# Optimization experiments

Measured on AMD Instinct MI355X. Metric: run time of the kernel, lower is better.

## Reference

```python
import jax, jax.numpy as jnp
import numpy as np

N, C, G, M, E = 100000, 8, 8, 32, 1600000
EPS = 1e-8


def setup_inputs() -> dict:
    key = jax.random.key(0)
    k1, k2, k3, k4, k5 = jax.random.split(key, 5)
    x = jax.random.randint(k1, (N,), 0, M)
    prev_h = jax.random.uniform(k2, (N, C, G), dtype=jnp.float32)
    edge_index = jax.random.randint(k3, (2, E), 0, N)
    Q_neigh = jax.random.normal(k4, (C, C, G), dtype=jnp.float32) * 1.25
    B = jax.random.normal(k5, (C, M, G), dtype=jnp.float32) * 1.25
    return {"x": x, "prev_h": prev_h, "edge_index": edge_index,
            "Q_neigh": Q_neigh, "B": B}


def reference(x, prev_h, edge_index, Q_neigh, B):
    n = prev_h.shape[0]
    # softmax reparameterization (vectorized over n_gen)
    Qs = jax.nn.softmax(Q_neigh, axis=0)          # [C, C, G], columns sum to 1 over dim 0
    Bs = jax.nn.softmax(B, axis=1)                # [C, M, G], rows sum to 1 over M

    dst, src = edge_index[0], edge_index[1]
    neigh = prev_h[src]                            # [E, C, G] gather
    summed = jax.ops.segment_sum(neigh, dst, num_segments=n)            # [N, C, G]
    counts = jax.ops.segment_sum(jnp.ones((src.shape[0],), prev_h.dtype), dst,
                                 num_segments=n)                        # [N]
    aggr = summed / jnp.maximum(counts, 1.0)[:, None, None]             # scatter-mean, 0 for isolated nodes

    B_nodes = jnp.transpose(Bs[:, x], (1, 0, 2))[:, :, None, :]         # [N, C, 1, G]
    unnorm = B_nodes * (Qs[None, :, :, :] * aggr[:, None, :, :]) + EPS  # [N, C, C, G]

    denom = unnorm.sum(axis=(1, 2), keepdims=True)                      # [N, 1, 1, G]
    posterior_il = unnorm / denom
    posterior_i = posterior_il.sum(axis=2)                              # [N, C, G]
    likelihood = jnp.log(jnp.squeeze(denom, (1, 2)))                    # [N, G]
    return likelihood, posterior_i
```

## Files before the change

kernel.cpp:

```cpp
#include <hip/hip_runtime.h>

#define C_    8
#define G_    8
#define CG    64
#define CAP   48
#define CELL  56
#define BSPAN 256
#define SBLK  256
#define CVT   160
#define BG    512
#define Z1    2048
#define Z2    2048
#define ZTOT  4096
#define EPSF  1e-8f

__device__ __forceinline__ unsigned short bf16rne(float v) {
    unsigned u = __float_as_uint(v);
    return (unsigned short)((u + 0x7FFFu + ((u >> 16) & 1u)) >> 16);
}
__device__ __forceinline__ float bf16tof(unsigned short h) {
    return __uint_as_float((unsigned)h << 16);
}

__device__ __forceinline__ void zsum_block(int zgid, const float* __restrict__ Bmat,
                                           float* __restrict__ Z, int M) {
    if (zgid >= ZTOT) return;
    __shared__ float zpart[4][8];
    int c = zgid & 7, bx = zgid >> 3;
    const float4* B4 = (const float4*)(Bmat + (size_t)c * M * G_);
    const int total4 = M * 2;
    int tid = bx * 256 + threadIdx.x;
    const int zstride = (ZTOT / 8) * 256;
    float a0 = 0.f, a1 = 0.f, a2 = 0.f, a3 = 0.f;
    for (int f = tid; f < total4; f += zstride) {
        float4 v = B4[f];
        a0 += __expf(v.x); a1 += __expf(v.y); a2 += __expf(v.z); a3 += __expf(v.w);
    }
    #pragma unroll
    for (int m = 2; m <= 32; m <<= 1) {
        a0 += __shfl_xor(a0, m, 64);
        a1 += __shfl_xor(a1, m, 64);
        a2 += __shfl_xor(a2, m, 64);
        a3 += __shfl_xor(a3, m, 64);
    }
    int lane = threadIdx.x & 63, w = threadIdx.x >> 6;
    if (lane < 2) {
        int g0 = lane * 4;
        zpart[w][g0 + 0] = a0; zpart[w][g0 + 1] = a1;
        zpart[w][g0 + 2] = a2; zpart[w][g0 + 3] = a3;
    }
    __syncthreads();
    if (threadIdx.x < 8) {
        float s = zpart[0][threadIdx.x] + zpart[1][threadIdx.x]
                + zpart[2][threadIdx.x] + zpart[3][threadIdx.x];
        atomicAdd(&Z[c * G_ + threadIdx.x], s);
    }
}

__global__ void k_d1(const int* __restrict__ ei, int E, int npart,
                     int* __restrict__ counts, int* __restrict__ staging,
                     const float* __restrict__ prev_h, unsigned short* __restrict__ ph16,
                     int N, const float* __restrict__ Qn, float* __restrict__ Qs,
                     const int* __restrict__ x, unsigned short* __restrict__ blog16,
                     const float* __restrict__ Bmat, float* __restrict__ Z, int M) {
    int b = blockIdx.x;
    if (b < SBLK) {
        __shared__ int cur[512];
        for (int p = threadIdx.x; p < npart; p += 256) cur[p] = 0;
        __syncthreads();
        int chunk = (E + SBLK - 1) / SBLK;
        int lo = b * chunk, hi = min(E, lo + chunk);
        for (int e = lo + threadIdx.x; e < hi; e += 256) {
            int dst = ei[e], src = ei[E + e];
            int p = dst >> 8;
            int c = atomicAdd(&cur[p], 1);
            if (c < CELL) staging[(p * SBLK + b) * CELL + c] = ((dst & 255) << 23) | src;
        }
        __syncthreads();
        for (int p = threadIdx.x; p < npart; p += 256)
            counts[p * SBLK + b] = cur[p];
    } else if (b < SBLK + CVT) {
        int gid = (b - SBLK) * 256 + threadIdx.x;
        int total8 = N * 8;
        const int cstride = CVT * 256;
        for (int f = gid; f < total8; f += cstride) {
            const float4* s = (const float4*)(prev_h + (size_t)f * 8);
            float4 v0 = s[0], v1 = s[1];
            float vv[8] = {v0.x, v0.y, v0.z, v0.w, v1.x, v1.y, v1.z, v1.w};
            unsigned r[4];
            #pragma unroll
            for (int k = 0; k < 4; ++k)
                r[k] = (unsigned)bf16rne(vv[2 * k]) | ((unsigned)bf16rne(vv[2 * k + 1]) << 16);
            *(uint4*)(ph16 + (size_t)f * 8) = make_uint4(r[0], r[1], r[2], r[3]);
        }
    } else if (b == SBLK + CVT) {
        __shared__ float e[512];
        __shared__ float cs[64];
        int t = threadIdx.x;
        e[t] = __expf(Qn[t]); e[t + 256] = __expf(Qn[t + 256]);
        __syncthreads();
        if (t < 64) {
            float s = 0.f;
            #pragma unroll
            for (int i2 = 0; i2 < 8; ++i2) s += e[i2 * 64 + t];
            cs[t] = s;
        }
        __syncthreads();
        Qs[t] = e[t] / cs[t & 63];
        Qs[t + 256] = e[t + 256] / cs[t & 63];
    } else if (b < SBLK + CVT + 1 + BG) {
        int gidx = b - (SBLK + CVT + 1);
        int lane = threadIdx.x & 63, w = threadIdx.x >> 6;
        int i = lane >> 3, g = lane & 7;
        const int step = BG * 4 * 4;
        for (int n0 = (gidx * 4 + w) * 4; n0 < N; n0 += step) {
            int xs[4];
            #pragma unroll
            for (int k = 0; k < 4; ++k) xs[k] = (n0 + k < N) ? x[n0 + k] : 0;
            #pragma unroll
            for (int k = 0; k < 4; ++k)
                if (n0 + k < N)
                    blog16[(size_t)(n0 + k) * CG + lane] =
                        bf16rne(Bmat[((size_t)i * M + xs[k]) * G_ + g]);
        }
    } else {
        zsum_block(b - (SBLK + CVT + 1 + BG), Bmat, Z, M);
    }
}

__global__ void k_d2(const int* __restrict__ counts, const int* __restrict__ staging,
                     int* __restrict__ cnt, int* __restrict__ csr, int N, int npart,
                     const float* __restrict__ Bmat, float* __restrict__ Z, int M) {
    int b = blockIdx.x;
    if (b >= npart) { zsum_block(Z1 + (b - npart), Bmat, Z, M); return; }
    __shared__ int cl[BSPAN];
    __shared__ int csl[BSPAN * CAP];
    int t = threadIdx.x;
    cl[t] = 0;
    __syncthreads();
    int cnum = min(counts[b * SBLK + t], CELL);
    int cbase = (b * SBLK + t) * CELL;
    for (int j = 0; j < cnum; ++j) {
        int v = staging[cbase + j];
        int local = (unsigned)v >> 23;
        int src = v & 0x7FFFFF;
        int pos = atomicAdd(&cl[local], 1);
        if (pos < CAP) csl[local * CAP + pos] = src;
    }
    __syncthreads();
    int n = b * BSPAN + t;
    if (n < N) cnt[n] = cl[t];
    for (int idx = t; idx < BSPAN * CAP; idx += 256)
        csr[(size_t)b * (BSPAN * CAP) + idx] = csl[idx];
}

__global__ void k_ti(const unsigned short* __restrict__ ph16, const int* __restrict__ cnt,
                     const int* __restrict__ csr, const float* __restrict__ Qs,
                     const unsigned short* __restrict__ blog16,
                     const float* __restrict__ Z, float* __restrict__ out, int N) {
    int lane = threadIdx.x & 63, w = threadIdx.x >> 6;
    int i = lane >> 3, g = lane & 7;
    int base = blockIdx.x * 16 + w * 4;
    if (base >= N) return;
    float invZ = 1.f / Z[lane];
    int nk[4]; bool valid[4]; int deg[4], dl[4], nb[4];
    #pragma unroll
    for (int k = 0; k < 4; ++k) {
        int n = base + k;
        valid[k] = (n < N);
        nk[k] = valid[k] ? n : (N - 1);
    }
    #pragma unroll
    for (int k = 0; k < 4; ++k) {
        deg[k] = valid[k] ? cnt[nk[k]] : 0;
        dl[k]  = min(deg[k], CAP);
        nb[k]  = dl[k] >> 2;
    }
    float q[8];
    #pragma unroll
    for (int l = 0; l < 8; ++l) q[l] = Qs[i * 64 + l * 8 + g];
    float acc[4] = {0.f, 0.f, 0.f, 0.f};
    int nbmax = max(max(nb[0], nb[1]), max(nb[2], nb[3]));
    for (int q2 = 0; q2 < nbmax; ++q2) {
        #pragma unroll
        for (int k = 0; k < 4; ++k) {
            if (q2 < nb[k]) {
                int4 s4 = ((const int4*)(csr + (size_t)nk[k] * CAP))[q2];
                acc[k] += bf16tof(ph16[(s4.x << 6) | lane]);
                acc[k] += bf16tof(ph16[(s4.y << 6) | lane]);
                acc[k] += bf16tof(ph16[(s4.z << 6) | lane]);
                acc[k] += bf16tof(ph16[(s4.w << 6) | lane]);
            }
        }
    }
    #pragma unroll
    for (int k = 0; k < 4; ++k) {
        const int* crow = csr + (size_t)nk[k] * CAP;
        for (int e2 = nb[k] * 4; e2 < dl[k]; ++e2)
            acc[k] += bf16tof(ph16[(crow[e2] << 6) | lane]);
    }
    #pragma unroll
    for (int k = 0; k < 4; ++k) {
        float aggr = (deg[k] > 0) ? acc[k] / (float)deg[k] : 0.f;
        float ti = 0.f;
        #pragma unroll
        for (int l = 0; l < 8; ++l) ti += q[l] * __shfl(aggr, l * 8 + g, 64);
        float bl = bf16tof(blog16[(size_t)nk[k] * CG + lane]);
        float u = __expf(bl) * invZ * ti;
        float s = u;
        #pragma unroll
        for (int m = 8; m <= 32; m <<= 1) s += __shfl_xor(s, m, 64);
        float denom = s + 64.f * EPSF;
        if (valid[k]) {
            if (i == 0) out[nk[k] * G_ + g] = logf(denom);
            out[(size_t)N * G_ + (size_t)nk[k] * CG + lane] = (u + 8.f * EPSF) / denom;
        }
    }
}

extern "C" void kernel_launch(void* const* d_in, const int* in_sizes, int n_in,
                              void* d_out, int out_size, void* d_ws, size_t ws_size,
                              hipStream_t stream) {
    const int*   x      = (const int*)d_in[0];
    const float* prev_h = (const float*)d_in[1];
    const int*   ei     = (const int*)d_in[2];
    const float* Qn     = (const float*)d_in[3];
    const float* Bm     = (const float*)d_in[4];
    float* out = (float*)d_out;

    int N = in_sizes[0];
    int E = in_sizes[2] / 2;
    int M = in_sizes[4] / CG;
    int npart = (N + BSPAN - 1) / BSPAN;
    int nAggr = (N + 15) / 16;

    float* Z      = (float*)d_ws;
    float* Qs     = Z + 64;
    int*   counts = (int*)d_ws + 576;
    int*   cnt    = counts + npart * SBLK;
    int*   stag   = cnt + N;
    int*   csr    = stag + (size_t)npart * SBLK * CELL;
    unsigned short* ph16   = (unsigned short*)(csr + (size_t)npart * BSPAN * CAP);
    unsigned short* blog16 = ph16 + (size_t)N * CG;

    hipMemsetAsync(d_ws, 0, 64 * sizeof(float), stream);

    k_d1<<<SBLK + CVT + 1 + BG + Z1, 256, 0, stream>>>(
        ei, E, npart, counts, stag, prev_h, ph16, N, Qn, Qs, x, blog16, Bm, Z, M);
    k_d2<<<npart + Z2, 256, 0, stream>>>(counts, stag, cnt, csr, N, npart, Bm, Z, M);
    k_ti<<<nAggr, 256, 0, stream>>>(ph16, cnt, csr, Qs, blog16, Z, out, N);
}
```

Before: 141.0 us.

## Pad CSR rows with a zero sentinel node to make gather loop branch-free

```diff
diff --git a/kernel.cpp b/kernel.cpp
--- a/kernel.cpp
+++ b/kernel.cpp
@@ -93,6 +93,8 @@
                 r[k] = (unsigned)bf16rne(vv[2 * k]) | ((unsigned)bf16rne(vv[2 * k + 1]) << 16);
             *(uint4*)(ph16 + (size_t)f * 8) = make_uint4(r[0], r[1], r[2], r[3]);
         }
+        if (b == SBLK && threadIdx.x < 64)
+            ph16[(size_t)N * CG + threadIdx.x] = 0;
     } else if (b == SBLK + CVT) {
         __shared__ float e[512];
         __shared__ float cs[64];
@@ -150,20 +152,24 @@
     __syncthreads();
     int n = b * BSPAN + t;
     if (n < N) cnt[n] = cl[t];
-    for (int idx = t; idx < BSPAN * CAP; idx += 256)
-        csr[(size_t)b * (BSPAN * CAP) + idx] = csl[idx];
-}
-
-__global__ void k_ti(const unsigned short* __restrict__ ph16, const int* __restrict__ cnt,
-                     const int* __restrict__ csr, const float* __restrict__ Qs,
-                     const unsigned short* __restrict__ blog16,
-                     const float* __restrict__ Z, float* __restrict__ out, int N) {
+    for (int idx = t; idx < BSPAN * CAP; idx += 256) {
+        int local = idx / CAP, pos = idx - local * CAP;
+        csr[(size_t)b * (BSPAN * CAP) + idx] =
+            (pos < min(cl[local], CAP)) ? csl[idx] : N;
+    }
+}
+
+__global__ void __launch_bounds__(128)
+k_ti(const unsigned short* __restrict__ ph16, const int* __restrict__ cnt,
+     const int* __restrict__ csr, const float* __restrict__ Qs,
+     const unsigned short* __restrict__ blog16,
+     const float* __restrict__ Z, float* __restrict__ out, int N) {
     int lane = threadIdx.x & 63, w = threadIdx.x >> 6;
     int i = lane >> 3, g = lane & 7;
-    int base = blockIdx.x * 16 + w * 4;
+    int base = blockIdx.x * 8 + w * 4;
     if (base >= N) return;
     float invZ = 1.f / Z[lane];
-    int nk[4]; bool valid[4]; int deg[4], dl[4], nb[4];
+    int nk[4]; bool valid[4]; int deg[4], ng[4];
     #pragma unroll
     for (int k = 0; k < 4; ++k) {
         int n = base + k;
@@ -173,31 +179,29 @@
     #pragma unroll
     for (int k = 0; k < 4; ++k) {
         deg[k] = valid[k] ? cnt[nk[k]] : 0;
-        dl[k]  = min(deg[k], CAP);
-        nb[k]  = dl[k] >> 2;
+        ng[k]  = (min(deg[k], CAP) + 3) >> 2;
     }
     float q[8];
     #pragma unroll
     for (int l = 0; l < 8; ++l) q[l] = Qs[i * 64 + l * 8 + g];
+    const unsigned short* phl = ph16 + lane;
     float acc[4] = {0.f, 0.f, 0.f, 0.f};
-    int nbmax = max(max(nb[0], nb[1]), max(nb[2], nb[3]));
-    for (int q2 = 0; q2 < nbmax; ++q2) {
+    int ngmax = max(max(ng[0], ng[1]), max(ng[2], ng[3]));
+    #pragma unroll 2
+    for (int q2 = 0; q2 < ngmax; ++q2) {
+        int4 s4[4];
         #pragma unroll
         for (int k = 0; k < 4; ++k) {
-            if (q2 < nb[k]) {
-                int4 s4 = ((const int4*)(csr + (size_t)nk[k] * CAP))[q2];
-                acc[k] += bf16tof(ph16[(s4.x << 6) | lane]);
-                acc[k] += bf16tof(ph16[(s4.y << 6) | lane]);
-                acc[k] += bf16tof(ph16[(s4.z << 6) | lane]);
-                acc[k] += bf16tof(ph16[(s4.w << 6) | lane]);
-            }
-        }
-    }
-    #pragma unroll
-    for (int k = 0; k < 4; ++k) {
-        const int* crow = csr + (size_t)nk[k] * CAP;
-        for (int e2 = nb[k] * 4; e2 < dl[k]; ++e2)
-            acc[k] += bf16tof(ph16[(crow[e2] << 6) | lane]);
+            int idx = min(q2, ng[k] > 0 ? ng[k] - 1 : 0);
+            s4[k] = ((const int4*)(csr + (size_t)nk[k] * CAP))[q2 < ng[k] ? q2 : (CAP / 4 - 1)];
+        }
+        #pragma unroll
+        for (int k = 0; k < 4; ++k) {
+            acc[k] += bf16tof(phl[(size_t)s4[k].x << 6]);
+            acc[k] += bf16tof(phl[(size_t)s4[k].y << 6]);
+            acc[k] += bf16tof(phl[(size_t)s4[k].z << 6]);
+            acc[k] += bf16tof(phl[(size_t)s4[k].w << 6]);
+        }
     }
     #pragma unroll
     for (int k = 0; k < 4; ++k) {
@@ -232,7 +236,6 @@
     int E = in_sizes[2] / 2;
     int M = in_sizes[4] / CG;
     int npart = (N + BSPAN - 1) / BSPAN;
-    int nAggr = (N + 15) / 16;
 
     float* Z      = (float*)d_ws;
     float* Qs     = Z + 64;
@@ -241,12 +244,12 @@
     int*   stag   = cnt + N;
     int*   csr    = stag + (size_t)npart * SBLK * CELL;
     unsigned short* ph16   = (unsigned short*)(csr + (size_t)npart * BSPAN * CAP);
-    unsigned short* blog16 = ph16 + (size_t)N * CG;
+    unsigned short* blog16 = ph16 + (size_t)(N + 1) * CG;
 
     hipMemsetAsync(d_ws, 0, 64 * sizeof(float), stream);
 
     k_d1<<<SBLK + CVT + 1 + BG + Z1, 256, 0, stream>>>(
         ei, E, npart, counts, stag, prev_h, ph16, N, Qn, Qs, x, blog16, Bm, Z, M);
     k_d2<<<npart + Z2, 256, 0, stream>>>(counts, stag, cnt, csr, N, npart, Bm, Z, M);
-    k_ti<<<nAggr, 256, 0, stream>>>(ph16, cnt, csr, Qs, blog16, Z, out, N);
-}
+    k_ti<<<(N + 7) / 8, 128, 0, stream>>>(ph16, cnt, csr, Qs, blog16, Z, out, N);
+}
```

Measured after the change: 139.4 us. Within noise of the previous version (-1.1%).
